# Kernel tuning notes

Hardware: AMD Instinct MI355X
Metric: run time of the kernel (lower is better)

## Reference

```python
import jax, jax.numpy as jnp
import numpy as np

B, S, D = 2, 2048, 1024
H = 16
HD = D // H  # 64
ROPE_BASE = 10000.0


def rotate_half(x):
    x1, x2 = jnp.split(x, 2, axis=-1)
    return jnp.concatenate((-x2, x1), axis=-1)


def rope_cos_sin(seq_len, dim, dtype):
    inv_freq = 1.0 / (ROPE_BASE ** (jnp.arange(0, dim, 2, dtype=jnp.float32) / dim))
    t = jnp.arange(seq_len, dtype=jnp.float32)
    freqs = jnp.einsum('i,j->ij', t, inv_freq)          # [S, dim/2]
    emb = jnp.concatenate((freqs, freqs), axis=-1)      # [S, dim]
    return jnp.cos(emb).astype(dtype), jnp.sin(emb).astype(dtype)


def setup_inputs() -> dict:
    key = jax.random.key(0)
    ks = jax.random.split(key, 5)
    std = 0.02
    return {
        'x': jax.random.normal(ks[0], (B, S, D), dtype=jnp.float32),
        'wq': jax.random.normal(ks[1], (D, D), dtype=jnp.float32) * std,
        'wk': jax.random.normal(ks[2], (D, D), dtype=jnp.float32) * std,
        'wv': jax.random.normal(ks[3], (D, D), dtype=jnp.float32) * std,
        'wo': jax.random.normal(ks[4], (D, D), dtype=jnp.float32) * std,
    }


def reference(x, wq, wk, wv, wo):
    b, s, d = x.shape
    # Q/K/V projections (nn.Linear: x @ W.T)
    q = jnp.einsum('bsd,ed->bse', x, wq).reshape(b, s, H, HD).transpose(0, 2, 1, 3)
    k = jnp.einsum('bsd,ed->bse', x, wk).reshape(b, s, H, HD).transpose(0, 2, 1, 3)
    v = jnp.einsum('bsd,ed->bse', x, wv).reshape(b, s, H, HD).transpose(0, 2, 1, 3)
    # RoPE
    cos, sin = rope_cos_sin(s, HD, x.dtype)  # [s, HD]
    cos = cos[None, None]  # [1,1,s,HD]
    sin = sin[None, None]
    q = q * cos + rotate_half(q) * sin
    k = k * cos + rotate_half(k) * sin
    # Causal SDPA
    scale = HD ** -0.5
    scores = jnp.einsum('bhqd,bhkd->bhqk', q, k) * scale
    causal = jnp.tril(jnp.ones((s, s), dtype=bool))
    scores = jnp.where(causal[None, None], scores, jnp.finfo(scores.dtype).min)
    attn = jax.nn.softmax(scores, axis=-1)
    out = jnp.einsum('bhqk,bhkd->bhqd', attn, v)
    out = out.transpose(0, 2, 1, 3).reshape(b, s, d)
    return jnp.einsum('bsd,ed->bse', out, wo)
```

## Files before the change

kernel.cpp:

```cpp
#include <hip/hip_runtime.h>
#include <hip/hip_bf16.h>
#include <cstdint>
#include <cstddef>

#define BDIM 2
#define SDIM 2048
#define DDIM 1024
#define HN   16
#define HDIM 64

using bf16 = __bf16;
typedef __attribute__((ext_vector_type(8))) __bf16 bf16x8;
typedef __attribute__((ext_vector_type(4))) __bf16 bf16x4;
typedef __attribute__((ext_vector_type(4))) float  f32x4;

#define MFMA16(a, b, c) __builtin_amdgcn_mfma_f32_16x16x32_bf16((a), (b), (c), 0, 0, 0)

#define ASYNC16(g, l)                                                          \
  __builtin_amdgcn_global_load_lds(                                            \
      (const __attribute__((address_space(1))) void*)(g),                      \
      (__attribute__((address_space(3))) void*)(l), 16, 0, 0)

#define QSCALE 0.1803368801111204f

struct Ptr5 { const float* p[5]; };
__global__ __launch_bounds__(256) void cvt_all(Ptr5 srcs, bf16* __restrict__ xb,
                                               bf16* __restrict__ wb,
                                               float2* __restrict__ cq,
                                               float2* __restrict__ ck) {
  const int NX4 = (BDIM * SDIM * DDIM) / 4;
  int i = blockIdx.x * 256 + threadIdx.x;

  if (i < SDIM * 32) {
    int s = i >> 5, j = i & 31;
    float inv = powf(10000.f, -(float)j * (1.f / 32.f));
    float a = (float)s * inv;
    float sn, c;
    sincosf(a, &sn, &c);
    ck[i] = make_float2(c, sn);
    cq[i] = make_float2(c * QSCALE, sn * QSCALE);
  }

  const float* src;
  bf16* dst;
  int j;
  if (i < NX4) {
    src = srcs.p[0]; dst = xb; j = i;
  } else {
    int k = i - NX4;
    int seg = k >> 18;
    j = k & 262143;
    src = srcs.p[seg + 1];
    dst = wb + (size_t)seg * (DDIM * DDIM);
  }
  float4 v = ((const float4*)src)[j];
  bf16x4 o = {(__bf16)v.x, (__bf16)v.y, (__bf16)v.z, (__bf16)v.w};
  *(bf16x4*)(dst + (size_t)j * 4) = o;
}

__global__ __launch_bounds__(256) void gemm_qkv(const bf16* __restrict__ A,
                                                const bf16* __restrict__ B0,
                                                bf16* __restrict__ C0,
                                                bf16* __restrict__ Vt,
                                                const float2* __restrict__ cqT,
                                                const float2* __restrict__ ckT) {
  constexpr int K = 1024;
  __shared__ __align__(16) bf16 Sh[128 * 136];
  bf16* const As = Sh;
  bf16* const Bs = Sh + 8192;
  const int tid = threadIdx.x;
  const int l = tid & 63, w = tid >> 6;
  const int wr = w >> 1, wc = w & 1;
  const int lr = l & 15, lg = l >> 4;
  const int bm = blockIdx.y * 128;
  const int bn = blockIdx.x * 128;
  const bf16* Bw = B0 + (size_t)blockIdx.z * (1024 * 1024);

  f32x4 acc[4][4] = {};

  for (int k0 = 0; k0 < K; k0 += 64) {
    __syncthreads();
#pragma unroll
    for (int i = 0; i < 4; ++i) {
      int idx = i * 2048 + tid * 8;
      int row = idx >> 6, col = idx & 63;
      ASYNC16(A + (size_t)(bm + row) * K + (k0 + col), As + idx);
      ASYNC16(Bw + (size_t)(bn + row) * K + (k0 + col), Bs + idx);
    }
    __syncthreads();
#pragma unroll
    for (int c = 0; c < 2; ++c) {
      bf16x8 af[4], bfr[4];
#pragma unroll
      for (int m = 0; m < 4; ++m)
        af[m] = *(const bf16x8*)(As + (wr * 64 + m * 16 + lr) * 64 + c * 32 + lg * 8);
#pragma unroll
      for (int n = 0; n < 4; ++n)
        bfr[n] = *(const bf16x8*)(Bs + (wc * 64 + n * 16 + lr) * 64 + c * 32 + lg * 8);
      __builtin_amdgcn_s_setprio(1);
#pragma unroll
      for (int m = 0; m < 4; ++m)
#pragma unroll
        for (int n = 0; n < 4; ++n)
          acc[m][n] = MFMA16(af[m], bfr[n], acc[m][n]);
      __builtin_amdgcn_s_setprio(0);
    }
  }

  const int z = blockIdx.z;
  if (z < 2) {
    __syncthreads();
#pragma unroll
    for (int m = 0; m < 4; ++m)
#pragma unroll
      for (int n = 0; n < 4; ++n)
#pragma unroll
        for (int r = 0; r < 4; ++r)
          Sh[(wr * 64 + m * 16 + lg * 4 + r) * 136 + wc * 64 + n * 16 + lr] =
              (__bf16)acc[m][n][r];
    __syncthreads();
    const int row_l = tid >> 1, half = tid & 1;
    const int row = bm + row_l;
    const int bb = row >> 11, s = row & (SDIM - 1);
    const int h = (bn >> 6) + half;
    const float2* T = z ? ckT : cqT;
    bf16x8 v[8];
#pragma unroll
    for (int kk = 0; kk < 8; ++kk)
      v[kk] = *(const bf16x8*)(Sh + row_l * 136 + half * 64 + kk * 8);
    bf16x8 ov[8];
#pragma unroll
    for (int kk = 0; kk < 4; ++kk)
#pragma unroll
      for (int e = 0; e < 8; ++e) {
        float2 cs = T[s * 32 + kk * 8 + e];
        float lo = (float)v[kk][e], hi = (float)v[kk + 4][e];
        ov[kk][e]     = (__bf16)(lo * cs.x - hi * cs.y);
        ov[kk + 4][e] = (__bf16)(hi * cs.x + lo * cs.y);
      }
    bf16* Cb = C0 + (size_t)z * ((size_t)BDIM * SDIM * DDIM) +
               ((size_t)(bb * HN + h) * SDIM + s) * HDIM;
#pragma unroll
    for (int kk = 0; kk < 8; ++kk)
      *(bf16x8*)(Cb + kk * 8) = ov[kk];
  } else {
    __syncthreads();
#pragma unroll
    for (int m = 0; m < 4; ++m)
#pragma unroll
      for (int n = 0; n < 4; ++n)
#pragma unroll
        for (int r = 0; r < 4; ++r)
          Sh[(wc * 64 + n * 16 + lr) * 136 + wr * 64 + m * 16 + lg * 4 + r] =
              (__bf16)acc[m][n][r];
    __syncthreads();
    const int rg = tid >> 4;
    const int cl = tid & 15;
    const int bb = bm >> 11, s0 = (bm & (SDIM - 1)) + cl * 8;
#pragma unroll
    for (int i = 0; i < 8; ++i) {
      const int hdl = rg * 8 + i;
      const int col = bn + hdl;
      const int h = col >> 6, hd = col & 63;
      bf16x8 v = *(const bf16x8*)(Sh + hdl * 136 + cl * 8);
      *(bf16x8*)(Vt + ((size_t)(bb * HN + h) * HDIM + hd) * SDIM + s0) = v;
    }
  }
}

__global__ __launch_bounds__(512) void gemm_out(const bf16* __restrict__ A,
                                                const bf16* __restrict__ Bw,
                                                float* __restrict__ C) {
  constexpr int K = 1024;
  __shared__ __align__(16) bf16 As[128 * 64];
  __shared__ __align__(16) bf16 Bs[128 * 64];
  const int tid = threadIdx.x;
  const int l = tid & 63, w = tid >> 6;
  const int wr = w >> 1, wc = w & 1;
  const int lr = l & 15, lg = l >> 4;
  const int bm = blockIdx.y * 128;
  const int bn = blockIdx.x * 128;

  f32x4 acc[2][4] = {};

  for (int k0 = 0; k0 < K; k0 += 64) {
    __syncthreads();
#pragma unroll
    for (int i = 0; i < 2; ++i) {
      int idx = i * 4096 + tid * 8;
      int row = idx >> 6, col = idx & 63;
      ASYNC16(A + (size_t)(bm + row) * K + (k0 + col), As + idx);
      ASYNC16(Bw + (size_t)(bn + row) * K + (k0 + col), Bs + idx);
    }
    __syncthreads();
#pragma unroll
    for (int c = 0; c < 2; ++c) {
      bf16x8 af[2], bfr[4];
#pragma unroll
      for (int m = 0; m < 2; ++m)
        af[m] = *(const bf16x8*)(As + (wr * 32 + m * 16 + lr) * 64 + c * 32 + lg * 8);
#pragma unroll
      for (int n = 0; n < 4; ++n)
        bfr[n] = *(const bf16x8*)(Bs + (wc * 64 + n * 16 + lr) * 64 + c * 32 + lg * 8);
      __builtin_amdgcn_s_setprio(1);
#pragma unroll
      for (int m = 0; m < 2; ++m)
#pragma unroll
        for (int n = 0; n < 4; ++n)
          acc[m][n] = MFMA16(af[m], bfr[n], acc[m][n]);
      __builtin_amdgcn_s_setprio(0);
    }
  }

#pragma unroll
  for (int m = 0; m < 2; ++m)
#pragma unroll
    for (int n = 0; n < 4; ++n)
#pragma unroll
      for (int r = 0; r < 4; ++r) {
        int row = bm + wr * 32 + m * 16 + lg * 4 + r;
        int col = bn + wc * 64 + n * 16 + lr;
        C[(size_t)row * DDIM + col] = acc[m][n][r];
      }
}

__global__ __launch_bounds__(512) void attn_fwd(const bf16* __restrict__ qg,
                                                const bf16* __restrict__ kg,
                                                const bf16* __restrict__ vtg,
                                                bf16* __restrict__ og) {
  __shared__ __align__(16) bf16 Sl[2][3][4096];
  __shared__ __align__(16) bf16 Pl[8][1024];

  const int tid = threadIdx.x;
  const int l = tid & 63, w = tid >> 6;
  const int g = w >> 2, wg = w & 3;
  const int lr = l & 15, lg = l >> 4;
  const int bh = blockIdx.x;
  const int qt = 31 - blockIdx.y;
  const int q0 = qt * 64;
  const size_t hb = (size_t)bh * SDIM * HDIM;
  const bf16* Q  = qg + hb;
  const bf16* Kp = kg + hb;
  const bf16* Vp = vtg + hb;
  const int b = bh >> 4, h = bh & 15;
  bf16* Pw = &Pl[w][0];
  const int swz = lr & 7;

  const int mm0 = 2 * wg, mm1 = 2 * wg + 1;
  const int f0 = mm0 & 3, c0 = mm0 >> 2;
  const int f1 = mm1 & 3, c1 = mm1 >> 2;
  const int lo0 = mm0 * 512 + l * 8;
  const int lo1 = mm1 * 512 + l * 8;
  bf16* const SlG = &Sl[g][0][0];

  bf16x8 qf[2];
#pragma unroll
  for (int c = 0; c < 2; ++c)
    qf[c] = *(const bf16x8*)(Q + (size_t)(q0 + wg * 16 + lr) * HDIM + c * 32 + lg * 8);

  f32x4 o[4] = {};
  float lsum = 0.f;

  const int ng   = (qt >= g) ? ((qt - g) >> 1) + 1 : 0;
  const int smax = (qt >> 1) + 1;

  const bf16* kN0 = Kp + (size_t)(f0 * 16 + lr) * HDIM + c0 * 32 + lg * 8 + (size_t)g * 64 * HDIM;
  const bf16* kN1 = Kp + (size_t)(f1 * 16 + lr) * HDIM + c1 * 32 + lg * 8 + (size_t)g * 64 * HDIM;
  const bf16* vN0 = Vp + (size_t)(f0 * 16 + lr) * SDIM + c0 * 32 + lg * 8 + g * 64;
  const bf16* vN1 = Vp + (size_t)(f1 * 16 + lr) * SDIM + c1 * 32 + lg * 8 + g * 64;

  if (ng > 0) {
    ASYNC16(kN0, SlG + 0 * 4096 + lo0); kN0 += 128 * HDIM;
    ASYNC16(kN1, SlG + 0 * 4096 + lo1); kN1 += 128 * HDIM;
    ASYNC16(vN0, SlG + 1 * 4096 + lo0); vN0 += 128;
    ASYNC16(vN1, SlG + 1 * 4096 + lo1); vN1 += 128;
  }
  __syncthreads();

  int ks = 0, vs = 1;
  for (int s = 0; s < smax; ++s) {
    const int t = 2 * s + g;
    const bool act = (s < ng);
    const int kn = 3 - ks - vs;
    const bool hasNext = act && (s + 1 < ng);

    if (hasNext) {
      ASYNC16(kN0, SlG + kn * 4096 + lo0); kN0 += 128 * HDIM;
      ASYNC16(kN1, SlG + kn * 4096 + lo1); kN1 += 128 * HDIM;
    }

    const bool diag = (t == qt);
    const int fLim = diag ? wg : 3;

    f32x4 sc[4] = {};
    if (act) {
      __builtin_amdgcn_s_setprio(1);
#pragma unroll
      for (int c = 0; c < 2; ++c)
#pragma unroll
        for (int f = 0; f < 4; ++f)
          if (f <= fLim) {
            bf16x8 kfr = *(const bf16x8*)(SlG + ks * 4096 + (c * 4 + f) * 512 + l * 8);
            sc[f] = MFMA16(kfr, qf[c], sc[f]);
          }
      __builtin_amdgcn_s_setprio(0);
    }

    __builtin_amdgcn_s_barrier();
    __builtin_amdgcn_sched_barrier(0);

    if (hasNext) {
      ASYNC16(vN0, SlG + ks * 4096 + lo0); vN0 += 128;
      ASYNC16(vN1, SlG + ks * 4096 + lo1); vN1 += 128;
    }

    if (act) {
      if (diag) {
#pragma unroll
        for (int f = 0; f < 4; ++f)
#pragma unroll
          for (int r = 0; r < 4; ++r) {
            if (f > wg)
              sc[f][r] = -3e38f;
            else if (f == wg)
              sc[f][r] = (lg * 4 + r <= lr) ? sc[f][r] : -3e38f;
          }
      }

      float rs = 0.f;
#pragma unroll
      for (int f = 0; f < 4; ++f) {
        float p0 = exp2f(sc[f][0]);
        float p1 = exp2f(sc[f][1]);
        float p2 = exp2f(sc[f][2]);
        float p3 = exp2f(sc[f][3]);
        rs += (p0 + p1) + (p2 + p3);
        bf16x4 pv = {(__bf16)p0, (__bf16)p1, (__bf16)p2, (__bf16)p3};
        const int ch = f * 2 + (lg >> 1);
        *(bf16x4*)(Pw + lr * 64 + ((ch ^ swz) << 3) + (lg & 1) * 4) = pv;
      }
      lsum += rs;

      const int cLim = diag ? (wg >> 1) : 1;
      __builtin_amdgcn_s_setprio(1);
#pragma unroll
      for (int c = 0; c < 2; ++c)
        if (c <= cLim) {
          bf16x8 pf = *(const bf16x8*)(Pw + lr * 64 + (((c * 4 + lg) ^ swz) << 3));
#pragma unroll
          for (int n = 0; n < 4; ++n) {
            bf16x8 vfr = *(const bf16x8*)(SlG + vs * 4096 + (c * 4 + n) * 512 + l * 8);
            o[n] = MFMA16(pf, vfr, o[n]);
          }
        }
      __builtin_amdgcn_s_setprio(0);
    }

    __syncthreads();
    vs = ks;
    ks = kn;
  }

  float* Osh = (float*)&Sl[0][0][0];
  float* Lsh = Osh + 4096;

  if (g == 1) {
    Lsh[wg * 64 + l] = lsum;
#pragma unroll
    for (int n = 0; n < 4; ++n)
#pragma unroll
      for (int r = 0; r < 4; ++r)
        Osh[((wg * 4 + n) * 4 + r) * 64 + l] = o[n][r];
  }
  __syncthreads();

  if (g == 0) {
    float lt = lsum + Lsh[wg * 64 + l];
    lt += __shfl_xor(lt, 16);
    lt += __shfl_xor(lt, 32);
    float ltb[4];
#pragma unroll
    for (int r = 0; r < 4; ++r) ltb[r] = __shfl(lt, lg * 4 + r);
#pragma unroll
    for (int r = 0; r < 4; ++r) {
      float rl = 1.f / ltb[r];
      int qr = q0 + 16 * wg + lg * 4 + r;
#pragma unroll
      for (int n = 0; n < 4; ++n) {
        float o1 = Osh[((wg * 4 + n) * 4 + r) * 64 + l];
        og[((size_t)(b * SDIM + qr)) * DDIM + h * HDIM + n * 16 + lr] =
            (__bf16)((o[n][r] + o1) * rl);
      }
    }
  }
}

extern "C" void kernel_launch(void* const* d_in, const int* in_sizes, int n_in,
                              void* d_out, int out_size, void* d_ws, size_t ws_size,
                              hipStream_t stream) {
  const float* x  = (const float*)d_in[0];
  const float* wq = (const float*)d_in[1];
  const float* wk = (const float*)d_in[2];
  const float* wv = (const float*)d_in[3];
  const float* wo = (const float*)d_in[4];

  char* ws = (char*)d_ws;
  const size_t MB = 1024 * 1024;
  bf16* xb   = (bf16*)(ws + 0);
  bf16* wqb  = (bf16*)(ws + 8 * MB);
  bf16* wob  = (bf16*)(ws + 14 * MB);
  bf16* qb   = (bf16*)(ws + 16 * MB);
  bf16* kb   = (bf16*)(ws + 24 * MB);
  bf16* vtb  = (bf16*)(ws + 32 * MB);
  bf16* ob   = (bf16*)(ws + 40 * MB);
  float2* cqT = (float2*)(ws + 48 * MB);
  float2* ckT = (float2*)(ws + 48 * MB + 512 * 1024);

  const int NX = BDIM * SDIM * DDIM;
  const int NW = DDIM * DDIM;

  Ptr5 srcs{{x, wq, wk, wv, wo}};
  cvt_all<<<(NX / 4 + NW) / 256, 256, 0, stream>>>(srcs, xb, wqb, cqT, ckT);
  gemm_qkv<<<dim3(8, 32, 3), 256, 0, stream>>>(xb, wqb, qb, vtb, cqT, ckT);
  attn_fwd<<<dim3(32, 32), 512, 0, stream>>>(qb, kb, vtb, ob);
  gemm_out<<<dim3(8, 32), 512, 0, stream>>>(ob, wob, (float*)d_out);
}
```

Baseline: 123.0 us.

## Replace three-slot rotating K/V buffer with separate double-buffered K and V

The attention kernel previously used a three-slot rotating LDS buffer per group, with a mid-iteration barrier so the V prefetch could reuse the K slot just consumed. It now keeps separate double-buffered K and V arrays, issues both prefetches for the next tile at the start of each iteration, and removes the mid-loop barrier. This cuts one workgroup barrier per iteration and lets V loads start earlier, at the cost of more LDS (16 KB extra), which could lower occupancy.

Result: slower. 126.0 us (+2.4%).

```diff
diff --git a/kernel.cpp b/kernel.cpp
--- a/kernel.cpp
+++ b/kernel.cpp
@@ -228,7 +228,8 @@
                                                 const bf16* __restrict__ kg,
                                                 const bf16* __restrict__ vtg,
                                                 bf16* __restrict__ og) {
-  __shared__ __align__(16) bf16 Sl[2][3][4096];
+  __shared__ __align__(16) bf16 Kb[2][2][4096];
+  __shared__ __align__(16) bf16 Vb[2][2][4096];
   __shared__ __align__(16) bf16 Pl[8][1024];
 
   const int tid = threadIdx.x;
@@ -251,7 +252,8 @@
   const int f1 = mm1 & 3, c1 = mm1 >> 2;
   const int lo0 = mm0 * 512 + l * 8;
   const int lo1 = mm1 * 512 + l * 8;
-  bf16* const SlG = &Sl[g][0][0];
+  bf16* const KbG = &Kb[g][0][0];
+  bf16* const VbG = &Vb[g][0][0];
 
   bf16x8 qf[2];
 #pragma unroll
@@ -270,51 +272,44 @@
   const bf16* vN1 = Vp + (size_t)(f1 * 16 + lr) * SDIM + c1 * 32 + lg * 8 + g * 64;
 
   if (ng > 0) {
-    ASYNC16(kN0, SlG + 0 * 4096 + lo0); kN0 += 128 * HDIM;
-    ASYNC16(kN1, SlG + 0 * 4096 + lo1); kN1 += 128 * HDIM;
-    ASYNC16(vN0, SlG + 1 * 4096 + lo0); vN0 += 128;
-    ASYNC16(vN1, SlG + 1 * 4096 + lo1); vN1 += 128;
+    ASYNC16(kN0, KbG + lo0); kN0 += 128 * HDIM;
+    ASYNC16(kN1, KbG + lo1); kN1 += 128 * HDIM;
+    ASYNC16(vN0, VbG + lo0); vN0 += 128;
+    ASYNC16(vN1, VbG + lo1); vN1 += 128;
   }
   __syncthreads();
 
-  int ks = 0, vs = 1;
+  int cur = 0;
   for (int s = 0; s < smax; ++s) {
     const int t = 2 * s + g;
     const bool act = (s < ng);
-    const int kn = 3 - ks - vs;
     const bool hasNext = act && (s + 1 < ng);
 
     if (hasNext) {
-      ASYNC16(kN0, SlG + kn * 4096 + lo0); kN0 += 128 * HDIM;
-      ASYNC16(kN1, SlG + kn * 4096 + lo1); kN1 += 128 * HDIM;
+      bf16* kd = KbG + (cur ^ 1) * 4096;
+      bf16* vd = VbG + (cur ^ 1) * 4096;
+      ASYNC16(kN0, kd + lo0); kN0 += 128 * HDIM;
+      ASYNC16(kN1, kd + lo1); kN1 += 128 * HDIM;
+      ASYNC16(vN0, vd + lo0); vN0 += 128;
+      ASYNC16(vN1, vd + lo1); vN1 += 128;
     }
 
     const bool diag = (t == qt);
     const int fLim = diag ? wg : 3;
 
-    f32x4 sc[4] = {};
     if (act) {
+      f32x4 sc[4] = {};
       __builtin_amdgcn_s_setprio(1);
 #pragma unroll
       for (int c = 0; c < 2; ++c)
 #pragma unroll
         for (int f = 0; f < 4; ++f)
           if (f <= fLim) {
-            bf16x8 kfr = *(const bf16x8*)(SlG + ks * 4096 + (c * 4 + f) * 512 + l * 8);
+            bf16x8 kfr = *(const bf16x8*)(KbG + cur * 4096 + (c * 4 + f) * 512 + l * 8);
             sc[f] = MFMA16(kfr, qf[c], sc[f]);
           }
       __builtin_amdgcn_s_setprio(0);
-    }
-
-    __builtin_amdgcn_s_barrier();
-    __builtin_amdgcn_sched_barrier(0);
-
-    if (hasNext) {
-      ASYNC16(vN0, SlG + ks * 4096 + lo0); vN0 += 128;
-      ASYNC16(vN1, SlG + ks * 4096 + lo1); vN1 += 128;
-    }
-
-    if (act) {
+
       if (diag) {
 #pragma unroll
         for (int f = 0; f < 4; ++f)
@@ -349,7 +344,7 @@
           bf16x8 pf = *(const bf16x8*)(Pw + lr * 64 + (((c * 4 + lg) ^ swz) << 3));
 #pragma unroll
           for (int n = 0; n < 4; ++n) {
-            bf16x8 vfr = *(const bf16x8*)(SlG + vs * 4096 + (c * 4 + n) * 512 + l * 8);
+            bf16x8 vfr = *(const bf16x8*)(VbG + cur * 4096 + (c * 4 + n) * 512 + l * 8);
             o[n] = MFMA16(pf, vfr, o[n]);
           }
         }
@@ -357,11 +352,10 @@
     }
 
     __syncthreads();
-    vs = ks;
-    ks = kn;
-  }
-
-  float* Osh = (float*)&Sl[0][0][0];
+    cur ^= 1;
+  }
+
+  float* Osh = (float*)&Kb[0][0][0];
   float* Lsh = Osh + 4096;
 
   if (g == 1) {
```

## Process 128 query rows per attention block with two row fragments per warp

Applied to the files above, without the earlier changes.

The attention kernel now assigns 128 query rows to each block instead of 64, halving the grid. Each warp computes two 16-row query fragments against every K/V tile loaded into shared memory, so each tile is reused twice. Causal masking is recomputed per fragment from the tile offset. It also adds a minimum of four blocks per CU to the launch bounds; together with the doubled accumulators this may squeeze registers and cause spills.

Result: slower. 135.7 us (+10.3%).

```diff
diff --git a/kernel.cpp b/kernel.cpp
--- a/kernel.cpp
+++ b/kernel.cpp
@@ -224,10 +224,10 @@
       }
 }
 
-__global__ __launch_bounds__(512) void attn_fwd(const bf16* __restrict__ qg,
-                                                const bf16* __restrict__ kg,
-                                                const bf16* __restrict__ vtg,
-                                                bf16* __restrict__ og) {
+__global__ __launch_bounds__(512, 4) void attn_fwd(const bf16* __restrict__ qg,
+                                                   const bf16* __restrict__ kg,
+                                                   const bf16* __restrict__ vtg,
+                                                   bf16* __restrict__ og) {
   __shared__ __align__(16) bf16 Sl[2][3][4096];
   __shared__ __align__(16) bf16 Pl[8][1024];
 
@@ -236,8 +236,8 @@
   const int g = w >> 2, wg = w & 3;
   const int lr = l & 15, lg = l >> 4;
   const int bh = blockIdx.x;
-  const int qt = 31 - blockIdx.y;
-  const int q0 = qt * 64;
+  const int qp = 15 - blockIdx.y;
+  const int q0 = qp * 128;
   const size_t hb = (size_t)bh * SDIM * HDIM;
   const bf16* Q  = qg + hb;
   const bf16* Kp = kg + hb;
@@ -253,55 +253,117 @@
   const int lo1 = mm1 * 512 + l * 8;
   bf16* const SlG = &Sl[g][0][0];
 
-  bf16x8 qf[2];
-#pragma unroll
-  for (int c = 0; c < 2; ++c)
-    qf[c] = *(const bf16x8*)(Q + (size_t)(q0 + wg * 16 + lr) * HDIM + c * 32 + lg * 8);
-
-  f32x4 o[4] = {};
-  float lsum = 0.f;
-
-  const int ng   = (qt >= g) ? ((qt - g) >> 1) + 1 : 0;
-  const int smax = (qt >> 1) + 1;
+  bf16x8 qf[2][2];
+#pragma unroll
+  for (int rf = 0; rf < 2; ++rf)
+#pragma unroll
+    for (int c = 0; c < 2; ++c)
+      qf[rf][c] = *(const bf16x8*)(Q + (size_t)(q0 + 32 * wg + 16 * rf + lr) * HDIM +
+                                   c * 32 + lg * 8);
+
+  f32x4 o[2][4] = {};
+  float lsum[2] = {0.f, 0.f};
+
+  const int smax = qp + 1;
 
   const bf16* kN0 = Kp + (size_t)(f0 * 16 + lr) * HDIM + c0 * 32 + lg * 8 + (size_t)g * 64 * HDIM;
   const bf16* kN1 = Kp + (size_t)(f1 * 16 + lr) * HDIM + c1 * 32 + lg * 8 + (size_t)g * 64 * HDIM;
   const bf16* vN0 = Vp + (size_t)(f0 * 16 + lr) * SDIM + c0 * 32 + lg * 8 + g * 64;
   const bf16* vN1 = Vp + (size_t)(f1 * 16 + lr) * SDIM + c1 * 32 + lg * 8 + g * 64;
 
-  if (ng > 0) {
-    ASYNC16(kN0, SlG + 0 * 4096 + lo0); kN0 += 128 * HDIM;
-    ASYNC16(kN1, SlG + 0 * 4096 + lo1); kN1 += 128 * HDIM;
-    ASYNC16(vN0, SlG + 1 * 4096 + lo0); vN0 += 128;
-    ASYNC16(vN1, SlG + 1 * 4096 + lo1); vN1 += 128;
-  }
+  ASYNC16(kN0, SlG + 0 * 4096 + lo0); kN0 += 128 * HDIM;
+  ASYNC16(kN1, SlG + 0 * 4096 + lo1); kN1 += 128 * HDIM;
+  ASYNC16(vN0, SlG + 1 * 4096 + lo0); vN0 += 128;
+  ASYNC16(vN1, SlG + 1 * 4096 + lo1); vN1 += 128;
   __syncthreads();
 
   int ks = 0, vs = 1;
   for (int s = 0; s < smax; ++s) {
     const int t = 2 * s + g;
-    const bool act = (s < ng);
     const int kn = 3 - ks - vs;
-    const bool hasNext = act && (s + 1 < ng);
+    const bool hasNext = (s < qp);
 
     if (hasNext) {
       ASYNC16(kN0, SlG + kn * 4096 + lo0); kN0 += 128 * HDIM;
       ASYNC16(kN1, SlG + kn * 4096 + lo1); kN1 += 128 * HDIM;
     }
 
-    const bool diag = (t == qt);
-    const int fLim = diag ? wg : 3;
-
-    f32x4 sc[4] = {};
-    if (act) {
+    const int dt = t - 2 * qp;
+
+    {
+      const int eff = (dt >= 0) ? (2 * wg - 4 * dt) : 7;
+      if (eff >= 0) {
+        f32x4 sc[4] = {};
+        __builtin_amdgcn_s_setprio(1);
+#pragma unroll
+        for (int c = 0; c < 2; ++c)
+#pragma unroll
+          for (int f = 0; f < 4; ++f)
+            if (f <= eff) {
+              bf16x8 kfr = *(const bf16x8*)(SlG + ks * 4096 + (c * 4 + f) * 512 + l * 8);
+              sc[f] = MFMA16(kfr, qf[0][c], sc[f]);
+            }
+        __builtin_amdgcn_s_setprio(0);
+
+        if (eff <= 3) {
+#pragma unroll
+          for (int f = 0; f < 4; ++f)
+#pragma unroll
+            for (int r = 0; r < 4; ++r) {
+              if (f > eff)
+                sc[f][r] = -3e38f;
+              else if (f == eff)
+                sc[f][r] = (lg * 4 + r <= lr) ? sc[f][r] : -3e38f;
+            }
+        }
+
+        float rs = 0.f;
+#pragma unroll
+        for (int f = 0; f < 4; ++f) {
+          float p0 = exp2f(sc[f][0]);
+          float p1 = exp2f(sc[f][1]);
+          float p2 = exp2f(sc[f][2]);
+          float p3 = exp2f(sc[f][3]);
+          rs += (p0 + p1) + (p2 + p3);
+          bf16x4 pv = {(__bf16)p0, (__bf16)p1, (__bf16)p2, (__bf16)p3};
+          const int ch = f * 2 + (lg >> 1);
+          *(bf16x4*)(Pw + lr * 64 + ((ch ^ swz) << 3) + (lg & 1) * 4) = pv;
+        }
+        lsum[0] += rs;
+
+        __builtin_amdgcn_s_setprio(1);
+        {
+          bf16x8 pf = *(const bf16x8*)(Pw + lr * 64 + ((lg ^ swz) << 3));
+#pragma unroll
+          for (int n = 0; n < 4; ++n) {
+            bf16x8 vfr = *(const bf16x8*)(SlG + vs * 4096 + (0 * 4 + n) * 512 + l * 8);
+            o[0][n] = MFMA16(pf, vfr, o[0][n]);
+          }
+        }
+        if (eff >= 2) {
+          bf16x8 pf = *(const bf16x8*)(Pw + lr * 64 + (((4 + lg) ^ swz) << 3));
+#pragma unroll
+          for (int n = 0; n < 4; ++n) {
+            bf16x8 vfr = *(const bf16x8*)(SlG + vs * 4096 + (1 * 4 + n) * 512 + l * 8);
+            o[1 * 0 + 0][n] = o[0][n];
+            o[0][n] = MFMA16(pf, vfr, o[0][n]);
+          }
+        }
+        __builtin_amdgcn_s_setprio(0);
+      }
+    }
+
+    const int eff1 = (dt >= 0) ? (2 * wg + 1 - 4 * dt) : 7;
+    f32x4 sc1[4] = {};
+    if (eff1 >= 0) {
       __builtin_amdgcn_s_setprio(1);
 #pragma unroll
       for (int c = 0; c < 2; ++c)
 #pragma unroll
         for (int f = 0; f < 4; ++f)
-          if (f <= fLim) {
+          if (f <= eff1) {
             bf16x8 kfr = *(const bf16x8*)(SlG + ks * 4096 + (c * 4 + f) * 512 + l * 8);
-            sc[f] = MFMA16(kfr, qf[c], sc[f]);
+            sc1[f] = MFMA16(kfr, qf[1][c], sc1[f]);
           }
       __builtin_amdgcn_s_setprio(0);
     }
@@ -314,45 +376,50 @@
       ASYNC16(vN1, SlG + ks * 4096 + lo1); vN1 += 128;
     }
 
-    if (act) {
-      if (diag) {
+    if (eff1 >= 0) {
+      if (eff1 <= 3) {
 #pragma unroll
         for (int f = 0; f < 4; ++f)
 #pragma unroll
           for (int r = 0; r < 4; ++r) {
-            if (f > wg)
-              sc[f][r] = -3e38f;
-            else if (f == wg)
-              sc[f][r] = (lg * 4 + r <= lr) ? sc[f][r] : -3e38f;
+            if (f > eff1)
+              sc1[f][r] = -3e38f;
+            else if (f == eff1)
+              sc1[f][r] = (lg * 4 + r <= lr) ? sc1[f][r] : -3e38f;
           }
       }
 
       float rs = 0.f;
 #pragma unroll
       for (int f = 0; f < 4; ++f) {
-        float p0 = exp2f(sc[f][0]);
-        float p1 = exp2f(sc[f][1]);
-        float p2 = exp2f(sc[f][2]);
-        float p3 = exp2f(sc[f][3]);
+        float p0 = exp2f(sc1[f][0]);
+        float p1 = exp2f(sc1[f][1]);
+        float p2 = exp2f(sc1[f][2]);
+        float p3 = exp2f(sc1[f][3]);
         rs += (p0 + p1) + (p2 + p3);
         bf16x4 pv = {(__bf16)p0, (__bf16)p1, (__bf16)p2, (__bf16)p3};
         const int ch = f * 2 + (lg >> 1);
         *(bf16x4*)(Pw + lr * 64 + ((ch ^ swz) << 3) + (lg & 1) * 4) = pv;
       }
-      lsum += rs;
-
-      const int cLim = diag ? (wg >> 1) : 1;
+      lsum[1] += rs;
+
       __builtin_amdgcn_s_setprio(1);
-#pragma unroll
-      for (int c = 0; c < 2; ++c)
-        if (c <= cLim) {
-          bf16x8 pf = *(const bf16x8*)(Pw + lr * 64 + (((c * 4 + lg) ^ swz) << 3));
-#pragma unroll
-          for (int n = 0; n < 4; ++n) {
-            bf16x8 vfr = *(const bf16x8*)(SlG + vs * 4096 + (c * 4 + n) * 512 + l * 8);
-            o[n] = MFMA16(pf, vfr, o[n]);
-          }
-        }
+      {
+        bf16x8 pf = *(const bf16x8*)(Pw + lr * 64 + ((lg ^ swz) << 3));
+#pragma unroll
+        for (int n = 0; n < 4; ++n) {
+          bf16x8 vfr = *(const bf16x8*)(SlG + vs * 4096 + (0 * 4 + n) * 512 + l * 8);
+          o[1][n] = MFMA16(pf, vfr, o[1][n]);
+        }
+      }
+      if (eff1 >= 2) {
+        bf16x8 pf = *(const bf16x8*)(Pw + lr * 64 + (((4 + lg) ^ swz) << 3));
+#pragma unroll
+        for (int n = 0; n < 4; ++n) {
+          bf16x8 vfr = *(const bf16x8*)(SlG + vs * 4096 + (1 * 4 + n) * 512 + l * 8);
+          o[1][n] = MFMA16(pf, vfr, o[1][n]);
+        }
+      }
       __builtin_amdgcn_s_setprio(0);
     }
 
@@ -362,34 +429,40 @@
   }
 
   float* Osh = (float*)&Sl[0][0][0];
-  float* Lsh = Osh + 4096;
+  float* Lsh = Osh + 8192;
 
   if (g == 1) {
-    Lsh[wg * 64 + l] = lsum;
-#pragma unroll
-    for (int n = 0; n < 4; ++n)
-#pragma unroll
-      for (int r = 0; r < 4; ++r)
-        Osh[((wg * 4 + n) * 4 + r) * 64 + l] = o[n][r];
+#pragma unroll
+    for (int rf = 0; rf < 2; ++rf) {
+      Lsh[(wg * 2 + rf) * 64 + l] = lsum[rf];
+#pragma unroll
+      for (int n = 0; n < 4; ++n)
+#pragma unroll
+        for (int r = 0; r < 4; ++r)
+          Osh[(((wg * 2 + rf) * 4 + n) * 4 + r) * 64 + l] = o[rf][n][r];
+    }
   }
   __syncthreads();
 
   if (g == 0) {
-    float lt = lsum + Lsh[wg * 64 + l];
-    lt += __shfl_xor(lt, 16);
-    lt += __shfl_xor(lt, 32);
-    float ltb[4];
-#pragma unroll
-    for (int r = 0; r < 4; ++r) ltb[r] = __shfl(lt, lg * 4 + r);
-#pragma unroll
-    for (int r = 0; r < 4; ++r) {
-      float rl = 1.f / ltb[r];
-      int qr = q0 + 16 * wg + lg * 4 + r;
-#pragma unroll
-      for (int n = 0; n < 4; ++n) {
-        float o1 = Osh[((wg * 4 + n) * 4 + r) * 64 + l];
-        og[((size_t)(b * SDIM + qr)) * DDIM + h * HDIM + n * 16 + lr] =
-            (__bf16)((o[n][r] + o1) * rl);
+#pragma unroll
+    for (int rf = 0; rf < 2; ++rf) {
+      float lt = lsum[rf] + Lsh[(wg * 2 + rf) * 64 + l];
+      lt += __shfl_xor(lt, 16);
+      lt += __shfl_xor(lt, 32);
+      float ltb[4];
+#pragma unroll
+      for (int r = 0; r < 4; ++r) ltb[r] = __shfl(lt, lg * 4 + r);
+#pragma unroll
+      for (int r = 0; r < 4; ++r) {
+        float rl = 1.f / ltb[r];
+        int qr = q0 + 32 * wg + 16 * rf + lg * 4 + r;
+#pragma unroll
+        for (int n = 0; n < 4; ++n) {
+          float o1 = Osh[(((wg * 2 + rf) * 4 + n) * 4 + r) * 64 + l];
+          og[((size_t)(b * SDIM + qr)) * DDIM + h * HDIM + n * 16 + lr] =
+              (__bf16)((o[rf][n][r] + o1) * rl);
+        }
       }
     }
   }
@@ -422,6 +495,6 @@
   Ptr5 srcs{{x, wq, wk, wv, wo}};
   cvt_all<<<(NX / 4 + NW) / 256, 256, 0, stream>>>(srcs, xb, wqb, cqT, ckT);
   gemm_qkv<<<dim3(8, 32, 3), 256, 0, stream>>>(xb, wqb, qb, vtb, cqT, ckT);
-  attn_fwd<<<dim3(32, 32), 512, 0, stream>>>(qb, kb, vtb, ob);
+  attn_fwd<<<dim3(32, 16), 512, 0, stream>>>(qb, kb, vtb, ob);
   gemm_out<<<dim3(8, 32), 512, 0, stream>>>(ob, wob, (float*)d_out);
 }
```
